# Optimization experiments

Hardware: AMD Instinct MI355X
Metric: run time of the kernel (lower is better)

Reference implementation:

```python
import jax, jax.numpy as jnp
import numpy as np

BRIGHTNESS_THRESHOLD = 0.4
NUM_BINS = 16


def _soft_histogram(x, mask):
    # x: [B, C, H, W], mask: [B, 1, H, W] (float 0/1)
    B, C, H, W = x.shape
    bin_centers = jnp.linspace(0.0, 1.0, NUM_BINS, dtype=x.dtype)  # [nb]
    bin_width = 1.0 / NUM_BINS
    inv_two_sigma2 = 1.0 / (2.0 * bin_width * bin_width)
    x_flat = x.reshape(B, C, H * W, 1)            # [B,C,HW,1]
    mask_flat = mask.reshape(B, 1, H * W, 1)      # [B,1,HW,1]
    weights = jnp.exp(-((x_flat - bin_centers) ** 2) * inv_two_sigma2)  # [B,C,HW,nb]
    hist = jnp.sum(weights * mask_flat, axis=2)   # [B,C,nb]
    hist = hist / (jnp.sum(hist, axis=-1, keepdims=True) + 1e-7)
    return hist


def setup_inputs() -> dict:
    key = jax.random.key(0)
    k1, k2 = jax.random.split(key)
    pred = jax.random.uniform(k1, (8, 3, 512, 512), dtype=jnp.float32)
    target = jax.random.uniform(k2, (8, 3, 512, 512), dtype=jnp.float32)
    return {"pred": pred, "target": target}


def reference(pred, target):
    target_brightness = jnp.mean(target, axis=1, keepdims=True)       # [B,1,H,W]
    bright_mask = (target_brightness > BRIGHTNESS_THRESHOLD).astype(pred.dtype)
    pred_hist = _soft_histogram(pred, bright_mask)
    target_hist = _soft_histogram(target, bright_mask)
    return jnp.mean(jnp.abs(pred_hist - target_hist))
```

## Files before the change

kernel.cpp:

```cpp
#include <hip/hip_runtime.h>

#define NB 16
#define BATCH 8
#define PLANE (512*512)
#define FBINS 512
#define CHUNKS 128
#define CTHREADS 512
#define PX_PER_BLOCK (PLANE / CHUNKS)
#define SLICES 8
#define FPB (FBINS / SLICES)

#if __has_builtin(__builtin_amdgcn_exp2f)
__device__ __forceinline__ float exp2_fast(float x) { return __builtin_amdgcn_exp2f(x); }
#else
__device__ __forceinline__ float exp2_fast(float x) { return __expf(x * 0.69314718056f); }
#endif

#define NEG_C2 (-0.8207331788f)

__device__ __forceinline__ int qbin(float x) {
    int f = (int)(x * (float)FBINS);
    return f > (FBINS - 1) ? (FBINS - 1) : f;
}

__global__ __launch_bounds__(CTHREADS, 8)
void count_kernel(const float* __restrict__ pred,
                  const float* __restrict__ tgt,
                  unsigned int* __restrict__ partial
                  )
{
    const int chunk = blockIdx.x;
    const int b     = blockIdx.y;
    const int tid   = threadIdx.x;

    __shared__ unsigned int cnt[3 * FBINS];
    #pragma unroll
    for (int k = 0; k < 3 * FBINS / CTHREADS; ++k)
        cnt[tid + k * CTHREADS] = 0u;
    __syncthreads();

    const float* pb = pred + (size_t)b * 3 * PLANE;
    const float* tb = tgt  + (size_t)b * 3 * PLANE;
    const int p = chunk * PX_PER_BLOCK + tid * 4;

    const float4 P0 = *(const float4*)(pb + p);
    const float4 P1 = *(const float4*)(pb + PLANE + p);
    const float4 P2 = *(const float4*)(pb + 2 * PLANE + p);
    const float4 T0 = *(const float4*)(tb + p);
    const float4 T1 = *(const float4*)(tb + PLANE + p);
    const float4 T2 = *(const float4*)(tb + 2 * PLANE + p);

    const float p0a[4] = {P0.x, P0.y, P0.z, P0.w};
    const float p1a[4] = {P1.x, P1.y, P1.z, P1.w};
    const float p2a[4] = {P2.x, P2.y, P2.z, P2.w};
    const float t0a[4] = {T0.x, T0.y, T0.z, T0.w};
    const float t1a[4] = {T1.x, T1.y, T1.z, T1.w};
    const float t2a[4] = {T2.x, T2.y, T2.z, T2.w};

    #pragma unroll
    for (int j = 0; j < 4; ++j) {
        const bool m = (t0a[j] + t1a[j] + t2a[j]) * (1.0f / 3.0f) > 0.4f;
        if (m) {
            atomicAdd(&cnt[           qbin(p0a[j])], 1u);
            atomicAdd(&cnt[           qbin(p1a[j])], 65536u);
            atomicAdd(&cnt[FBINS    + qbin(p2a[j])], 1u);
            atomicAdd(&cnt[FBINS    + qbin(t0a[j])], 65536u);
            atomicAdd(&cnt[2*FBINS  + qbin(t1a[j])], 1u);
            atomicAdd(&cnt[2*FBINS  + qbin(t2a[j])], 65536u);
        }
    }
    __syncthreads();

    #pragma unroll
    for (int k = 0; k < 3 * FBINS / CTHREADS; ++k) {
        const int w  = tid + k * CTHREADS;
        const int h2 = w >> 9;
        const int f  = w & (FBINS - 1);
        partial[(((size_t)h2 * BATCH + b) * CHUNKS + chunk) * FBINS + f] = cnt[w];
    }
}

__global__ __launch_bounds__(256)
void combine_kernel(const unsigned int* __restrict__ partial,
                    float* __restrict__ out2 )
{
    const int slice = blockIdx.x;
    const int hb    = blockIdx.y;
    const int h     = hb / BATCH;
    const int b     = hb % BATCH;
    const int h2    = h >> 1;
    const int sh    = (h & 1) * 16;
    const int tid   = threadIdx.x;

    const int f_loc = tid & (FPB - 1);
    const int q     = tid >> 6;
    const int f     = slice * FPB + f_loc;

    const unsigned int* base =
        partial + (((size_t)h2 * BATCH + b) * CHUNKS + q * 32) * FBINS + f;
    unsigned int s = 0u;
    #pragma unroll 8
    for (int c = 0; c < 32; ++c)
        s += (base[(size_t)c * FBINS] >> sh) & 0xFFFFu;

    __shared__ unsigned int red[4][FPB];
    red[q][f_loc] = s;
    __syncthreads();

    if (tid < FPB) {
        const float cf = (float)(red[0][tid] + red[1][tid] + red[2][tid] + red[3][tid]);
        const float y  = ((float)(slice * FPB + tid) + 0.5f) * (15.0f / (float)FBINS);

        float acc[NB];
        #pragma unroll
        for (int i = 0; i < NB; ++i) {
            const float u = y - (float)i;
            acc[i] = cf * exp2_fast(u * u * NEG_C2);
        }
        #pragma unroll
        for (int off = 32; off > 0; off >>= 1)
            #pragma unroll
            for (int i = 0; i < NB; ++i)
                acc[i] += __shfl_down(acc[i], off, 64);

        if (tid == 0) {
            float* o = out2 + ((size_t)slice * 48 + hb) * NB;
            #pragma unroll
            for (int i = 0; i < NB; ++i) o[i] = acc[i];
        }
    }
}

__global__ void finalize_kernel(const float* __restrict__ out2,
                                float* __restrict__ out)
{
    const int t = threadIdx.x;
    __shared__ float H[48 * NB];

    for (int e = t; e < 48 * NB; e += 384) {
        float v = 0.0f;
        #pragma unroll
        for (int s = 0; s < SLICES; ++s)
            v += out2[(size_t)s * 48 * NB + e];
        H[e] = v;
    }
    __syncthreads();

    const int b   = t / 48;
    const int rem = t % 48;
    const int c   = rem / NB;
    const int i   = rem % NB;

    const float* hp = H + ((c    ) * BATCH + b) * NB;
    const float* ht = H + ((c + 3) * BATCH + b) * NB;
    float sp = 0.0f, st = 0.0f;
    #pragma unroll
    for (int k = 0; k < NB; ++k) { sp += hp[k]; st += ht[k]; }

    float val = fabsf(hp[i] / (sp + 1e-7f) - ht[i] / (st + 1e-7f));

    #pragma unroll
    for (int off = 32; off > 0; off >>= 1)
        val += __shfl_down(val, off, 64);

    __shared__ float r[6];
    const int lane = t & 63, wv = t >> 6;
    if (lane == 0) r[wv] = val;
    __syncthreads();
    if (t == 0)
        out[0] = (r[0] + r[1] + r[2] + r[3] + r[4] + r[5]) * (1.0f / 384.0f);
}

extern "C" void kernel_launch(void* const* d_in, const int* in_sizes, int n_in,
                              void* d_out, int out_size, void* d_ws, size_t ws_size,
                              hipStream_t stream)
{
    const float* pred = (const float*)d_in[0];
    const float* tgt  = (const float*)d_in[1];

    unsigned int* partial = (unsigned int*)d_ws;
    float* out2 = (float*)((char*)d_ws + (size_t)3 * BATCH * CHUNKS * FBINS * 4);

    count_kernel<<<dim3(CHUNKS, BATCH), CTHREADS, 0, stream>>>(pred, tgt, partial);
    combine_kernel<<<dim3(SLICES, 48), 256, 0, stream>>>(partial, out2);
    finalize_kernel<<<1, 384, 0, stream>>>(out2, (float*)d_out);
}
```

Before: 90.60 us.

## Combine both packed 16-bit halves per block and parallelize Gaussian bin expansion

The combine kernel now runs one block per packed partial plane (24 instead of 48). Each word is read once and both 16-bit halves are accumulated, instead of two separate blocks each re-reading the word for one half. The Gaussian expansion to 16 bins is spread across all 512 threads (each thread handles one bin and four fine bins), replacing the single wave with a 16-register accumulator and a long shuffle chain. This halves global reads of the partial buffer and shortens the serial tail, at the cost of fewer, larger blocks and an extra shared-memory reduction stage.

```diff
diff --git a/kernel.cpp b/kernel.cpp
--- a/kernel.cpp
+++ b/kernel.cpp
@@ -80,16 +80,12 @@
     }
 }
 
-__global__ __launch_bounds__(256)
+__global__ __launch_bounds__(512)
 void combine_kernel(const unsigned int* __restrict__ partial,
                     float* __restrict__ out2 )
 {
     const int slice = blockIdx.x;
-    const int hb    = blockIdx.y;
-    const int h     = hb / BATCH;
-    const int b     = hb % BATCH;
-    const int h2    = h >> 1;
-    const int sh    = (h & 1) * 16;
+    const int pb    = blockIdx.y;
     const int tid   = threadIdx.x;
 
     const int f_loc = tid & (FPB - 1);
@@ -97,37 +93,57 @@
     const int f     = slice * FPB + f_loc;
 
     const unsigned int* base =
-        partial + (((size_t)h2 * BATCH + b) * CHUNKS + q * 32) * FBINS + f;
-    unsigned int s = 0u;
-    #pragma unroll 8
-    for (int c = 0; c < 32; ++c)
-        s += (base[(size_t)c * FBINS] >> sh) & 0xFFFFu;
-
-    __shared__ unsigned int red[4][FPB];
-    red[q][f_loc] = s;
-    __syncthreads();
-
-    if (tid < FPB) {
-        const float cf = (float)(red[0][tid] + red[1][tid] + red[2][tid] + red[3][tid]);
-        const float y  = ((float)(slice * FPB + tid) + 0.5f) * (15.0f / (float)FBINS);
-
-        float acc[NB];
-        #pragma unroll
-        for (int i = 0; i < NB; ++i) {
-            const float u = y - (float)i;
-            acc[i] = cf * exp2_fast(u * u * NEG_C2);
-        }
-        #pragma unroll
-        for (int off = 32; off > 0; off >>= 1)
-            #pragma unroll
-            for (int i = 0; i < NB; ++i)
-                acc[i] += __shfl_down(acc[i], off, 64);
-
-        if (tid == 0) {
-            float* o = out2 + ((size_t)slice * 48 + hb) * NB;
-            #pragma unroll
-            for (int i = 0; i < NB; ++i) o[i] = acc[i];
-        }
+        partial + ((size_t)pb * CHUNKS + q * 16) * FBINS + f;
+    unsigned int slo = 0u, shi = 0u;
+    #pragma unroll
+    for (int c = 0; c < 16; ++c) {
+        const unsigned int v = base[(size_t)c * FBINS];
+        slo += v & 0xFFFFu;
+        shi += v >> 16;
+    }
+
+    __shared__ float red_lo[8][FPB];
+    __shared__ float red_hi[8][FPB];
+    red_lo[q][f_loc] = (float)slo;
+    red_hi[q][f_loc] = (float)shi;
+    __syncthreads();
+
+    const int i    = tid & 15;
+    const int fg   = (tid >> 4) & 15;
+    const int half = tid >> 8;
+
+    float val = 0.0f;
+    #pragma unroll
+    for (int k = 0; k < 4; ++k) {
+        const int fl = fg * 4 + k;
+        float c;
+        if (half == 0)
+            c = red_lo[0][fl] + red_lo[1][fl] + red_lo[2][fl] + red_lo[3][fl]
+              + red_lo[4][fl] + red_lo[5][fl] + red_lo[6][fl] + red_lo[7][fl];
+        else
+            c = red_hi[0][fl] + red_hi[1][fl] + red_hi[2][fl] + red_hi[3][fl]
+              + red_hi[4][fl] + red_hi[5][fl] + red_hi[6][fl] + red_hi[7][fl];
+        const float y = ((float)(slice * FPB + fl) + 0.5f) * (15.0f / (float)FBINS);
+        const float u = y - (float)i;
+        val += c * exp2_fast(u * u * NEG_C2);
+    }
+
+    val += __shfl_xor(val, 16, 64);
+    val += __shfl_xor(val, 32, 64);
+
+    __shared__ float acc[8][NB];
+    if ((tid & 63) < 16) acc[tid >> 6][i] = val;
+    __syncthreads();
+
+    if (tid < 32) {
+        const int hf = tid >> 4;
+        const int ii = tid & 15;
+        const int w0 = hf * 4;
+        const float v = acc[w0][ii] + acc[w0+1][ii] + acc[w0+2][ii] + acc[w0+3][ii];
+        const int h2 = pb >> 3;
+        const int b  = pb & 7;
+        const int h  = h2 * 2 + hf;
+        out2[((size_t)slice * 48 + h * BATCH + b) * NB + ii] = v;
     }
 }
 
@@ -182,6 +198,6 @@
     float* out2 = (float*)((char*)d_ws + (size_t)3 * BATCH * CHUNKS * FBINS * 4);
 
     count_kernel<<<dim3(CHUNKS, BATCH), CTHREADS, 0, stream>>>(pred, tgt, partial);
-    combine_kernel<<<dim3(SLICES, 48), 256, 0, stream>>>(partial, out2);
+    combine_kernel<<<dim3(SLICES, 24), 512, 0, stream>>>(partial, out2);
     finalize_kernel<<<1, 384, 0, stream>>>(out2, (float*)d_out);
 }
```

Result: no change. 90.09 us (median of 2 runs) (-0.6%).
